# Kernel optimization log

Hardware: AMD Instinct MI355X
Metric: run time of the kernel (lower is better)

The kernel has to match this reference:

```python
import jax, jax.numpy as jnp
import numpy as np

# ---- VoronoiDecoder constants (defaults from __init__) ----
EPS = 1e-8
W_MIN = 0.005
BETA = 0.02
RAW_TEMP = 5.0
H_MIN, H_MAX = 0.5, 2.0
J_BETA_SCALE = 1.0
J_WIDTH_BONUS = 0.15
J_KEFF_LAMBDA = 0.05
J_KEFF_K0 = 3.0
J_KEFF_S = 0.35
J_TRIPLE_LAMBDA = 0.15
J_TRIPLE_POWER = 1.5
GAP_THR_MIN, GAP_THR_MAX = 0.0, 0.5
BIG_THR_MIN, BIG_THR_MAX = 0.0, 0.6
ALPHA_MIN, ALPHA_MAX = 0.01, 0.2
ETA_MIN, ETA_MAX = 0.01, 0.2


def _map_raw(x, lo, hi):
    return lo + (hi - lo) * jax.nn.sigmoid(x)


def _forward(uv, seeds_raw, w_raw, h_raw, theta, a_raw,
             gap_thr_raw, big_thr_raw, alpha_raw, eta_raw):
    seeds = seeds_raw                                   # (S,2); seeds_uv is identity
    # pairwise seed distance (default buffers: single non-periodic face -> plain norm)
    v = seeds[:, None, :] - seeds[None, :, :]           # (S,S,2)
    pair_dist = jnp.sqrt(jnp.sum(v * v, axis=-1) + EPS)
    # width(): geometric clamp + sigmoid blend, symmetrized
    w_max_pair = jnp.maximum(0.8 * pair_dist, W_MIN + EPS)
    w_geo = W_MIN + (w_max_pair - W_MIN) * jax.nn.sigmoid(w_raw / RAW_TEMP)
    W = 0.5 * (w_geo + w_geo.T)                         # (S,S)
    # height(): bounded sigmoid
    h = H_MIN + (H_MAX - H_MIN) * jax.nn.sigmoid(h_raw[0])
    # anisotropic metric per seed: rotate by theta, scale by aspect a
    diff = uv[:, None, :] - seeds[None, :, :]           # (Q,S,2)
    c, s = jnp.cos(theta), jnp.sin(theta)               # (S,)
    du = c * diff[..., 0] + s * diff[..., 1]
    dv = -s * diff[..., 0] + c * diff[..., 1]
    a = 0.5 + 1.5 * jax.nn.sigmoid(a_raw)               # (S,) aspect ratio in (0.5,2)
    d = jnp.sqrt((du * a) ** 2 + (dv / a) ** 2 + EPS)   # (Q,S)
    # nearest / second-nearest seed (soft Voronoi wall field)
    neg2, idx2 = jax.lax.top_k(-d, 2)                   # (Q,2)
    d1 = -neg2[:, 0]
    d2 = -neg2[:, 1]
    gap = d2 - d1
    w_pair = W[idx2[:, 0], idx2[:, 1]]                  # (Q,)
    # junction gating via soft effective seed count keff
    p = jax.nn.softmax(-d / BETA, axis=-1)              # (Q,S)
    keff = 1.0 / (jnp.sum(p * p, axis=-1) + EPS)
    jfac = jax.nn.sigmoid((keff - J_KEFF_K0) / J_KEFF_S)
    w_eff = w_pair * (1.0 + J_WIDTH_BONUS * jfac)
    beta_eff = BETA * J_BETA_SCALE * (1.0 + J_KEFF_LAMBDA * jfac)
    wall = jax.nn.sigmoid((w_eff - gap) / beta_eff)
    # pair gating (use_pair_gating=True): suppress walls across large gaps
    gap_thr = _map_raw(gap_thr_raw[0], GAP_THR_MIN, GAP_THR_MAX)
    big_thr = _map_raw(big_thr_raw[0], BIG_THR_MIN, BIG_THR_MAX)
    alpha_g = _map_raw(alpha_raw[0], ALPHA_MIN, ALPHA_MAX)
    eta_g = _map_raw(eta_raw[0], ETA_MIN, ETA_MAX)
    gate = jax.nn.sigmoid((gap_thr - gap) / alpha_g) * jax.nn.sigmoid((big_thr - d1) / eta_g)
    # triple-junction bonus density
    triple = J_TRIPLE_LAMBDA * jnp.maximum(keff - J_KEFF_K0, 0.0) ** J_TRIPLE_POWER
    occ = jnp.clip(wall * gate + triple, 0.0, 1.0)
    return occ * h                                      # (Q,) thickness field


def setup_inputs() -> dict:
    key = jax.random.key(0)
    ks = jax.random.split(key, 10)
    Q, S = 65536, 512
    return {
        "uv": jax.random.uniform(ks[0], (Q, 2), dtype=jnp.float32),
        "seeds_raw": jax.random.uniform(ks[1], (S, 2), dtype=jnp.float32),
        "w_raw": jax.random.normal(ks[2], (S, S), dtype=jnp.float32),
        "h_raw": jax.random.normal(ks[3], (1,), dtype=jnp.float32),
        "theta": jax.random.normal(ks[4], (S,), dtype=jnp.float32),
        "a_raw": jax.random.normal(ks[5], (S,), dtype=jnp.float32),
        "gap_thr_raw": jax.random.normal(ks[6], (1,), dtype=jnp.float32),
        "big_thr_raw": jax.random.normal(ks[7], (1,), dtype=jnp.float32),
        "alpha_raw": jax.random.normal(ks[8], (1,), dtype=jnp.float32),
        "eta_raw": jax.random.normal(ks[9], (1,), dtype=jnp.float32),
    }


def reference(uv, seeds_raw, w_raw, h_raw, theta, a_raw,
              gap_thr_raw, big_thr_raw, alpha_raw, eta_raw):
    return _forward(uv, seeds_raw, w_raw, h_raw, theta, a_raw,
                    gap_thr_raw, big_thr_raw, alpha_raw, eta_raw)
```

## Files before the change

kernel.cpp:

```cpp
#include <hip/hip_runtime.h>
#include <math.h>

#define EPSF    1e-8f
#define W_MINF  0.005f
#define BETAF   0.02f
#define LOG2E   1.4426950408889634f

constexpr double KD    = 1.4426950408889634 / 0.02;
constexpr float  K2F   = (float)(KD * KD);
constexpr float  K2EPS = (float)(KD * KD * 1e-8);
constexpr float  INVK  = (float)(1.0 / KD);

typedef float v2f __attribute__((ext_vector_type(2)));

__device__ __forceinline__ float fast_exp(float x) {
    return __builtin_amdgcn_exp2f(x * LOG2E);
}
__device__ __forceinline__ float sigm(float x) {
    return 1.0f / (1.0f + fast_exp(-x));
}
__device__ __forceinline__ float ex2(float x) { return __builtin_amdgcn_exp2f(x); }

__device__ __forceinline__ unsigned min3u(unsigned a, unsigned b, unsigned c) {
    unsigned d;
    asm("v_min3_u32 %0, %1, %2, %3" : "=v"(d) : "v"(a), "v"(b), "v"(c));
    return d;
}
__device__ __forceinline__ unsigned med3u(unsigned a, unsigned b, unsigned c) {
    unsigned d;
    asm("v_med3_u32 %0, %1, %2, %3" : "=v"(d) : "v"(a), "v"(b), "v"(c));
    return d;
}

extern "C" __global__ __launch_bounds__(512)
void seed_prep(const float* __restrict__ seeds,
               const float* __restrict__ theta,
               const float* __restrict__ a_raw,
               float* __restrict__ ws, int S)
{
    int j = blockIdx.x * blockDim.x + threadIdx.x;
    if (j >= S) return;
    float sx = seeds[2 * j + 0];
    float sy = seeds[2 * j + 1];
    float sn, cs;
    __sincosf(theta[j], &sn, &cs);
    float a   = 0.5f + 1.5f * sigm(a_raw[j]);
    float a2  = a * a;
    float ia2 = 1.0f / a2;
    float c2 = cs * cs, s2 = sn * sn;
    ws[0 * 512 + j] = K2F * (c2 * a2 + s2 * ia2);
    ws[1 * 512 + j] = K2F * (s2 * a2 + c2 * ia2);
    ws[2 * 512 + j] = K2F * (cs * sn * (a2 - ia2));
    ws[3 * 512 + j] = sx;
    ws[4 * 512 + j] = sy;
}

extern "C" __global__ __launch_bounds__(512, 8)
void voronoi_kernel(const float* __restrict__ uv,
                    const float* __restrict__ w_raw,
                    const float* __restrict__ h_raw,
                    const float* __restrict__ gap_thr_raw,
                    const float* __restrict__ big_thr_raw,
                    const float* __restrict__ alpha_raw,
                    const float* __restrict__ eta_raw,
                    const float* __restrict__ ws,
                    float* __restrict__ out,
                    int Q, int S)
{
    __shared__ float sA[512], sB[512], sC[512], sX[512], sY[512];
    __shared__ unsigned mv1[8][64], mv2[8][64];
    __shared__ float    ms1[8][64], ms2[8][64];

    const int tid = threadIdx.x;
    {
        sA[tid] = ws[0 * 512 + tid];
        sB[tid] = ws[1 * 512 + tid];
        sC[tid] = ws[2 * 512 + tid];
        sX[tid] = ws[3 * 512 + tid];
        sY[tid] = ws[4 * 512 + tid];
    }
    __syncthreads();

    const int part = __builtin_amdgcn_readfirstlane((int)(tid >> 6));
    const int lane = tid & 63;
    const int q    = blockIdx.x * 64 + lane;
    const int qc   = q < Q ? q : (Q - 1);

    const float2 u = *reinterpret_cast<const float2*>(&uv[2 * qc]);
    const v2f uxv  = { u.x, u.x };
    const v2f uyv  = { u.y, u.y };
    const v2f epsv = { K2EPS, K2EPS };

    unsigned v1u = 0x7F7FFFFFu, v2u = 0x7F7FFFFFu;
    v2f s1v = { 0.0f, 0.0f };
    v2f s2v = { 0.0f, 0.0f };

    const int base = part * 64;
    #pragma unroll 4
    for (int t = 0; t < 64; t += 2) {
        const int j = base + t;
        const v2f A  = *reinterpret_cast<const v2f*>(&sA[j]);
        const v2f B  = *reinterpret_cast<const v2f*>(&sB[j]);
        const v2f C  = *reinterpret_cast<const v2f*>(&sC[j]);
        const v2f sx = *reinterpret_cast<const v2f*>(&sX[j]);
        const v2f sy = *reinterpret_cast<const v2f*>(&sY[j]);

        v2f dx = uxv - sx;
        v2f dy = uyv - sy;
        v2f p  = A * dx + C * dy;
        v2f qv = C * dx + B * dy;
        v2f r  = dx * p + (dy * qv + epsv);

        float e0 = ex2(-__builtin_amdgcn_sqrtf(r.x));
        float e1 = ex2(-__builtin_amdgcn_sqrtf(r.y));
        v2f e = { e0, e1 };
        s1v = s1v + e;
        s2v = e * e + s2v;

        unsigned pv0 = (__float_as_uint(r.x) & 0xFFFFFE00u) | (unsigned)j;
        unsigned pv1 = (__float_as_uint(r.y) & 0xFFFFFE00u) | (unsigned)(j + 1);
        unsigned m2  = med3u(v1u, pv0, pv1);
        v1u = min3u(v1u, pv0, pv1);
        v2u = v2u < m2 ? v2u : m2;
    }

    float s1 = s1v.x + s1v.y;
    float s2 = s2v.x + s2v.y;

    mv1[part][lane] = v1u;  mv2[part][lane] = v2u;
    ms1[part][lane] = s1;   ms2[part][lane] = s2;
    __syncthreads();
    if (part != 0) return;

    unsigned V1 = mv1[0][lane], V2 = mv2[0][lane];
    float    S1 = ms1[0][lane], S2 = ms2[0][lane];
    #pragma unroll
    for (int p2 = 1; p2 < 8; ++p2) {
        unsigned w1 = mv1[p2][lane], w2 = mv2[p2][lane];
        S1 += ms1[p2][lane];
        S2 += ms2[p2][lane];
        unsigned n1 = V1 < w1 ? V1 : w1;
        unsigned hi = V1 > w1 ? V1 : w1;
        unsigned l2 = V2 < w2 ? V2 : w2;
        V2 = hi < l2 ? hi : l2;
        V1 = n1;
    }

    const int i1 = (int)(V1 & 511u);
    const int i2 = (int)(V2 & 511u);
    float d1K = __builtin_amdgcn_sqrtf(__uint_as_float(V1));
    float d2K = __builtin_amdgcn_sqrtf(__uint_as_float(V2));
    float d1  = d1K * INVK;
    float gap = (d2K - d1K) * INVK;

    float sp2  = (S2 / S1) / S1;
    float keff = 1.0f / (sp2 + EPSF);
    float jfac = sigm((keff - 3.0f) * (1.0f / 0.35f));

    float ddx   = sX[i1] - sX[i2];
    float ddy   = sY[i1] - sY[i2];
    float pdist = __builtin_amdgcn_sqrtf(fmaf(ddx, ddx, fmaf(ddy, ddy, EPSF)));
    float wmax  = fmaxf(0.8f * pdist, W_MINF + EPSF);
    float sij   = sigm(w_raw[i1 * S + i2] * 0.2f);
    float sji   = sigm(w_raw[i2 * S + i1] * 0.2f);
    float wpair = W_MINF + (wmax - W_MINF) * 0.5f * (sij + sji);

    float weff     = wpair * fmaf(0.15f, jfac, 1.0f);
    float beta_eff = BETAF * fmaf(0.05f, jfac, 1.0f);
    float wall     = sigm((weff - gap) / beta_eff);

    float gap_thr = 0.5f  * sigm(gap_thr_raw[0]);
    float big_thr = 0.6f  * sigm(big_thr_raw[0]);
    float alpha_g = 0.01f + 0.19f * sigm(alpha_raw[0]);
    float eta_g   = 0.01f + 0.19f * sigm(eta_raw[0]);

    float gate = sigm((gap_thr - gap) / alpha_g) * sigm((big_thr - d1) / eta_g);

    float t      = fmaxf(keff - 3.0f, 0.0f);
    float triple = 0.15f * t * __builtin_amdgcn_sqrtf(t);

    float h   = 0.5f + 1.5f * sigm(h_raw[0]);
    float occ = fminf(fmaxf(fmaf(wall, gate, triple), 0.0f), 1.0f);
    if (q < Q) out[q] = occ * h;
}

extern "C" void kernel_launch(void* const* d_in, const int* in_sizes, int n_in,
                              void* d_out, int out_size, void* d_ws, size_t ws_size,
                              hipStream_t stream)
{
    const float* uv          = (const float*)d_in[0];
    const float* seeds_raw   = (const float*)d_in[1];
    const float* w_raw       = (const float*)d_in[2];
    const float* h_raw       = (const float*)d_in[3];
    const float* theta       = (const float*)d_in[4];
    const float* a_raw       = (const float*)d_in[5];
    const float* gap_thr_raw = (const float*)d_in[6];
    const float* big_thr_raw = (const float*)d_in[7];
    const float* alpha_raw   = (const float*)d_in[8];
    const float* eta_raw     = (const float*)d_in[9];
    float* out = (float*)d_out;
    float* ws  = (float*)d_ws;

    const int Q = in_sizes[0] / 2;
    const int S = in_sizes[4];

    seed_prep<<<dim3((S + 511) / 512), dim3(512), 0, stream>>>(seeds_raw, theta,
                                                               a_raw, ws, S);

    dim3 block(512);
    dim3 grid((Q + 63) / 64);
    voronoi_kernel<<<grid, block, 0, stream>>>(uv, w_raw, h_raw,
                                               gap_thr_raw, big_thr_raw,
                                               alpha_raw, eta_raw,
                                               ws, out, Q, S);
}
```

Baseline: 88.99 us.

## Fuse seed preprocessing into main kernel and interleave seed params in LDS

```diff
diff --git a/kernel.cpp b/kernel.cpp
--- a/kernel.cpp
+++ b/kernel.cpp
@@ -12,6 +12,7 @@
 constexpr float  INVK  = (float)(1.0 / KD);
 
 typedef float v2f __attribute__((ext_vector_type(2)));
+typedef float v4f __attribute__((ext_vector_type(4)));
 
 __device__ __forceinline__ float fast_exp(float x) {
     return __builtin_amdgcn_exp2f(x * LOG2E);
@@ -32,52 +33,41 @@
     return d;
 }
 
-extern "C" __global__ __launch_bounds__(512)
-void seed_prep(const float* __restrict__ seeds,
-               const float* __restrict__ theta,
-               const float* __restrict__ a_raw,
-               float* __restrict__ ws, int S)
-{
-    int j = blockIdx.x * blockDim.x + threadIdx.x;
-    if (j >= S) return;
-    float sx = seeds[2 * j + 0];
-    float sy = seeds[2 * j + 1];
-    float sn, cs;
-    __sincosf(theta[j], &sn, &cs);
-    float a   = 0.5f + 1.5f * sigm(a_raw[j]);
-    float a2  = a * a;
-    float ia2 = 1.0f / a2;
-    float c2 = cs * cs, s2 = sn * sn;
-    ws[0 * 512 + j] = K2F * (c2 * a2 + s2 * ia2);
-    ws[1 * 512 + j] = K2F * (s2 * a2 + c2 * ia2);
-    ws[2 * 512 + j] = K2F * (cs * sn * (a2 - ia2));
-    ws[3 * 512 + j] = sx;
-    ws[4 * 512 + j] = sy;
-}
-
 extern "C" __global__ __launch_bounds__(512, 8)
 void voronoi_kernel(const float* __restrict__ uv,
+                    const float* __restrict__ seeds,
+                    const float* __restrict__ theta,
+                    const float* __restrict__ a_raw,
                     const float* __restrict__ w_raw,
                     const float* __restrict__ h_raw,
                     const float* __restrict__ gap_thr_raw,
                     const float* __restrict__ big_thr_raw,
                     const float* __restrict__ alpha_raw,
                     const float* __restrict__ eta_raw,
-                    const float* __restrict__ ws,
                     float* __restrict__ out,
                     int Q, int S)
 {
-    __shared__ float sA[512], sB[512], sC[512], sX[512], sY[512];
+    __shared__ float sg[256 * 12];
     __shared__ unsigned mv1[8][64], mv2[8][64];
     __shared__ float    ms1[8][64], ms2[8][64];
 
     const int tid = threadIdx.x;
     {
-        sA[tid] = ws[0 * 512 + tid];
-        sB[tid] = ws[1 * 512 + tid];
-        sC[tid] = ws[2 * 512 + tid];
-        sX[tid] = ws[3 * 512 + tid];
-        sY[tid] = ws[4 * 512 + tid];
+        const int j = tid;
+        float sx = seeds[2 * j + 0];
+        float sy = seeds[2 * j + 1];
+        float sn, cs;
+        __sincosf(theta[j], &sn, &cs);
+        float a   = 0.5f + 1.5f * sigm(a_raw[j]);
+        float a2  = a * a;
+        float ia2 = 1.0f / a2;
+        float c2 = cs * cs, s2 = sn * sn;
+        float* p = &sg[(j >> 1) * 12 + (j & 1)];
+        p[0] = K2F * (c2 * a2 + s2 * ia2);
+        p[2] = K2F * (s2 * a2 + c2 * ia2);
+        p[4] = K2F * (cs * sn * (a2 - ia2));
+        p[6] = sx;
+        p[8] = sy;
     }
     __syncthreads();
 
@@ -95,30 +85,34 @@
     v2f s1v = { 0.0f, 0.0f };
     v2f s2v = { 0.0f, 0.0f };
 
-    const int base = part * 64;
-    #pragma unroll 4
-    for (int t = 0; t < 64; t += 2) {
-        const int j = base + t;
-        const v2f A  = *reinterpret_cast<const v2f*>(&sA[j]);
-        const v2f B  = *reinterpret_cast<const v2f*>(&sB[j]);
-        const v2f C  = *reinterpret_cast<const v2f*>(&sC[j]);
-        const v2f sx = *reinterpret_cast<const v2f*>(&sX[j]);
-        const v2f sy = *reinterpret_cast<const v2f*>(&sY[j]);
-
-        v2f dx = uxv - sx;
-        v2f dy = uyv - sy;
-        v2f p  = A * dx + C * dy;
-        v2f qv = C * dx + B * dy;
-        v2f r  = dx * p + (dy * qv + epsv);
+    const int gbase = part * 32;
+    #pragma unroll 8
+    for (int g = 0; g < 32; ++g) {
+        const float* pp = &sg[(gbase + g) * 12];
+        const v4f r0 = *reinterpret_cast<const v4f*>(pp + 0);
+        const v4f r1 = *reinterpret_cast<const v4f*>(pp + 4);
+        const v2f r2 = *reinterpret_cast<const v2f*>(pp + 8);
+        const v2f A = { r0.x, r0.y };
+        const v2f B = { r0.z, r0.w };
+        const v2f C = { r1.x, r1.y };
+        const v2f X = { r1.z, r1.w };
+
+        v2f dx = uxv - X;
+        v2f dy = uyv - r2;
+        v2f p  = __builtin_elementwise_fma(A, dx, C * dy);
+        v2f qv = __builtin_elementwise_fma(C, dx, B * dy);
+        v2f r  = __builtin_elementwise_fma(
+                     dx, p, __builtin_elementwise_fma(dy, qv, epsv));
 
         float e0 = ex2(-__builtin_amdgcn_sqrtf(r.x));
         float e1 = ex2(-__builtin_amdgcn_sqrtf(r.y));
         v2f e = { e0, e1 };
         s1v = s1v + e;
-        s2v = e * e + s2v;
-
-        unsigned pv0 = (__float_as_uint(r.x) & 0xFFFFFE00u) | (unsigned)j;
-        unsigned pv1 = (__float_as_uint(r.y) & 0xFFFFFE00u) | (unsigned)(j + 1);
+        s2v = __builtin_elementwise_fma(e, e, s2v);
+
+        const int j0 = (gbase + g) * 2;
+        unsigned pv0 = (__float_as_uint(r.x) & 0xFFFFFE00u) | (unsigned)j0;
+        unsigned pv1 = (__float_as_uint(r.y) & 0xFFFFFE00u) | (unsigned)(j0 + 1);
         unsigned m2  = med3u(v1u, pv0, pv1);
         v1u = min3u(v1u, pv0, pv1);
         v2u = v2u < m2 ? v2u : m2;
@@ -157,8 +151,12 @@
     float keff = 1.0f / (sp2 + EPSF);
     float jfac = sigm((keff - 3.0f) * (1.0f / 0.35f));
 
-    float ddx   = sX[i1] - sX[i2];
-    float ddy   = sY[i1] - sY[i2];
+    float x1 = sg[(i1 >> 1) * 12 + 6 + (i1 & 1)];
+    float y1 = sg[(i1 >> 1) * 12 + 8 + (i1 & 1)];
+    float x2 = sg[(i2 >> 1) * 12 + 6 + (i2 & 1)];
+    float y2 = sg[(i2 >> 1) * 12 + 8 + (i2 & 1)];
+    float ddx   = x1 - x2;
+    float ddy   = y1 - y2;
     float pdist = __builtin_amdgcn_sqrtf(fmaf(ddx, ddx, fmaf(ddy, ddy, EPSF)));
     float wmax  = fmaxf(0.8f * pdist, W_MINF + EPSF);
     float sij   = sigm(w_raw[i1 * S + i2] * 0.2f);
@@ -199,18 +197,15 @@
     const float* alpha_raw   = (const float*)d_in[8];
     const float* eta_raw     = (const float*)d_in[9];
     float* out = (float*)d_out;
-    float* ws  = (float*)d_ws;
 
     const int Q = in_sizes[0] / 2;
     const int S = in_sizes[4];
 
-    seed_prep<<<dim3((S + 511) / 512), dim3(512), 0, stream>>>(seeds_raw, theta,
-                                                               a_raw, ws, S);
-
     dim3 block(512);
     dim3 grid((Q + 63) / 64);
-    voronoi_kernel<<<grid, block, 0, stream>>>(uv, w_raw, h_raw,
+    voronoi_kernel<<<grid, block, 0, stream>>>(uv, seeds_raw, theta, a_raw,
+                                               w_raw, h_raw,
                                                gap_thr_raw, big_thr_raw,
                                                alpha_raw, eta_raw,
-                                               ws, out, Q, S);
-}
+                                               out, Q, S);
+}
```

Result: faster. 86.93 us (-2.3%).
